# Optimization experiments

Measured on AMD Instinct MI355X. Metric: run time of the kernel, lower is better.

The kernel has to match this reference:

```python
import jax, jax.numpy as jnp
import numpy as np


def setup_inputs() -> dict:
    key = jax.random.key(0)
    k1, k2 = jax.random.split(key)
    N, DIM = 32768, 1024
    M, K, D = 8, 1024, 128  # n_quantizer, n_codeword, sub_dim
    x = jax.random.normal(k1, (N, DIM), dtype=jnp.float32)
    CodeBooks = jax.random.uniform(k2, (M, K, D), dtype=jnp.float32)  # torch.rand init
    return {"x": x, "CodeBooks": CodeBooks, "soft_rate": -1}


def reference(x, CodeBooks, soft_rate):
    # x: [N, dim]; CodeBooks: [M, K, D] with dim = M*D
    N = x.shape[0]
    M, K, D = CodeBooks.shape
    # forward detaches x before quantizing
    sx = jax.lax.stop_gradient(x).reshape(-1, M, D)  # [N, M, D]
    # squared euclidean distances for all sub-quantizers at once:
    # d2[n,m,k] = ||sx[n,m] - CB[m,k]||^2
    dots = jnp.einsum("nmd,mkd->nmk", sx, CodeBooks)          # [N, M, K]
    x2 = jnp.sum(sx * sx, axis=-1)                             # [N, M]
    c2 = jnp.sum(CodeBooks * CodeBooks, axis=-1)               # [M, K]
    d2 = x2[:, :, None] + c2[None, :, :] - 2.0 * dots          # [N, M, K]
    if soft_rate == -1:
        # argmax of -dist == argmin of squared dist (sqrt is monotone)
        idx = jnp.argmin(d2, axis=-1)                          # [N, M]
        Q = CodeBooks[jnp.arange(M)[None, :], idx]             # [N, M, D]
    else:
        dist = -jnp.sqrt(jnp.maximum(d2, 0.0))                 # -cdist, p=2
        w = jax.nn.softmax(dist * soft_rate, axis=-1)          # [N, M, K]
        Q = jnp.einsum("nmk,mkd->nmd", w, CodeBooks)           # [N, M, D]
    return Q.reshape(N, M * D)
```

## Files before the change

kernel.cpp:

```cpp
#include <hip/hip_runtime.h>
#include <stdint.h>

#define NROWS   32768
#define XDIM    1024
#define NCB     8
#define NCODE   1024
#define CDIM    128

#define CHUNK   32
#define NCHUNK  (NCODE / CHUNK)

#define NTH     256
#define ROWS_PB 128
#define RPW     32

typedef _Float16 h8 __attribute__((ext_vector_type(8)));
typedef float    f4 __attribute__((ext_vector_type(4)));

#define LO_SCALE 2048.0f
#define LO_INV   4.8828125e-4f

#define WS_HI   ((size_t)0)
#define WS_LO   ((size_t)NCB * NCODE * CDIM * 2)
#define WS_C2   ((size_t)2 * NCB * NCODE * CDIM * 2)
#define WS_NEED (WS_C2 + (size_t)NCB * NCODE * 4)

__device__ __forceinline__ void gload_lds16(const void* g, void* l) {
    __builtin_amdgcn_global_load_lds(
        (const __attribute__((address_space(1))) void*)g,
        (__attribute__((address_space(3))) void*)l, 16, 0, 0);
}

__global__ __launch_bounds__(256)
void precompute_kernel(const float* __restrict__ cb, uint8_t* __restrict__ ws)
{
    _Float16* hi = (_Float16*)(ws + WS_HI);
    _Float16* lo = (_Float16*)(ws + WS_LO);
    float*    c2 = (float*)(ws + WS_C2);

    const int idx  = blockIdx.x * 256 + threadIdx.x;
    const int g    = idx & 15;
    const int code = idx >> 4;
    const int kr   = code & 31;
    const int gs   = g ^ (kr & 7);

    const float* src = cb + (size_t)code * CDIM + gs * 8;
    float v[8];
    *(f4*)&v[0] = *(const f4*)src;
    *(f4*)&v[4] = *(const f4*)(src + 4);

    _Float16 hh[8], ll[8];
    double s = 0.0;
    #pragma unroll
    for (int i = 0; i < 8; ++i) {
        _Float16 h = (_Float16)v[i];
        float    r = v[i] - (float)h;
        hh[i] = h; ll[i] = (_Float16)(r * LO_SCALE);
        s = fma((double)v[i], (double)v[i], s);
    }
    const size_t off = (size_t)code * CDIM + g * 8;
    *(h8*)(hi + off) = *(h8*)hh;
    *(h8*)(lo + off) = *(h8*)ll;

    #pragma unroll
    for (int mask = 1; mask <= 8; mask <<= 1)
        s += __shfl_xor(s, mask, 16);
    if (g == 0) c2[code] = (float)s;
}

__global__ __launch_bounds__(NTH, 4)
void quant_fast(const float* __restrict__ x, const float* __restrict__ cb,
                const uint8_t* __restrict__ ws, float* __restrict__ out)
{
    __shared__ __align__(16) _Float16 chS[2][CHUNK][CDIM];
    __shared__ __align__(16) _Float16 clS[2][CHUNK][CDIM];
    __shared__ float  c2s[NCODE];
    __shared__ double x2p[2][ROWS_PB];
    __shared__ float  x2s[ROWS_PB];
    __shared__ int    idxs[ROWS_PB];

    const _Float16* pre_hi = (const _Float16*)(ws + WS_HI);
    const _Float16* pre_lo = (const _Float16*)(ws + WS_LO);
    const float*    c2w    = (const float*)(ws + WS_C2);

    const int t    = threadIdx.x;
    const int bid  = blockIdx.x;
    const int m    = bid >> 8;
    const int rb   = bid & 255;
    const int row0 = rb * ROWS_PB;

    const int l    = t & 63;
    const int w    = t >> 6;
    const int l15  = l & 15;
    const int lh   = l >> 4;
    const int mskr = (l & 7) * 8;

    *(f4*)&c2s[t * 4] = *(const f4*)&c2w[m * NCODE + t * 4];

    {
        const int row = t >> 1, q = t & 1;
        const float* p = x + (size_t)(row0 + row) * XDIM + m * CDIM + q * 64;
        double s0 = 0, s1 = 0;
        for (int i = 0; i < 64; i += 2) {
            double v0 = p[i], v1 = p[i + 1];
            s0 = fma(v0, v0, s0); s1 = fma(v1, v1, s1);
        }
        x2p[q][row] = s0 + s1;
    }

    h8 xh[2][4], xl[2][4];
    #pragma unroll
    for (int rs = 0; rs < 2; ++rs) {
        const float* xp = x + (size_t)(row0 + w * RPW + rs * 16 + l15) * XDIM + m * CDIM + lh * 8;
        #pragma unroll
        for (int ks = 0; ks < 4; ++ks) {
            float v[8];
            *(f4*)&v[0] = *(const f4*)(xp + ks * 32);
            *(f4*)&v[4] = *(const f4*)(xp + ks * 32 + 4);
            #pragma unroll
            for (int i = 0; i < 8; ++i) {
                _Float16 h = (_Float16)v[i];
                float    r = v[i] - (float)h;
                xh[rs][ks][i] = h;
                xl[rs][ks][i] = (_Float16)(r * LO_SCALE);
            }
        }
    }

    const size_t cbase = (size_t)m * NCODE * CDIM;
    auto stage = [&](int c, int buf) {
        const _Float16* gh = pre_hi + cbase + (size_t)(c * CHUNK + w * 8) * CDIM + l * 8;
        const _Float16* gl = pre_lo + cbase + (size_t)(c * CHUNK + w * 8) * CDIM + l * 8;
        gload_lds16(gh,            &chS[buf][w * 8][0]);
        gload_lds16(gh + 4 * CDIM, &chS[buf][w * 8 + 4][0]);
        gload_lds16(gl,            &clS[buf][w * 8][0]);
        gload_lds16(gl + 4 * CDIM, &clS[buf][w * 8 + 4][0]);
    };

    stage(0, 0);
    __syncthreads();
    if (t < ROWS_PB) x2s[t] = (float)(x2p[0][t] + x2p[1][t]);
    __syncthreads();

    float x2r[2][4];
    #pragma unroll
    for (int rs = 0; rs < 2; ++rs)
        #pragma unroll
        for (int j = 0; j < 4; ++j)
            x2r[rs][j] = x2s[w * RPW + rs * 16 + lh * 4 + j];

    float mval[2][4];
    int   midx[2][4];
    #pragma unroll
    for (int rs = 0; rs < 2; ++rs)
        #pragma unroll
        for (int j = 0; j < 4; ++j) { mval[rs][j] = 3.0e38f; midx[rs][j] = 0; }

    for (int c = 0; c < NCHUNK; ++c) {
        const int cur = c & 1;
        if (c + 1 < NCHUNK) stage(c + 1, cur ^ 1);

        #pragma unroll
        for (int cf = 0; cf < 2; ++cf) {
            const int kloc = cf * 16 + l15;
            f4 accH[2] = {{0,0,0,0},{0,0,0,0}};
            f4 accS[2] = {{0,0,0,0},{0,0,0,0}};
            #pragma unroll
            for (int ks = 0; ks < 4; ++ks) {
                const int e = (ks * 32 + lh * 8) ^ mskr;
                h8 bh = *(const h8*)&chS[cur][kloc][e];
                h8 bl = *(const h8*)&clS[cur][kloc][e];
                accH[0] = __builtin_amdgcn_mfma_f32_16x16x32_f16(xh[0][ks], bh, accH[0], 0, 0, 0);
                accH[1] = __builtin_amdgcn_mfma_f32_16x16x32_f16(xh[1][ks], bh, accH[1], 0, 0, 0);
                accS[0] = __builtin_amdgcn_mfma_f32_16x16x32_f16(xh[0][ks], bl, accS[0], 0, 0, 0);
                accS[0] = __builtin_amdgcn_mfma_f32_16x16x32_f16(xl[0][ks], bh, accS[0], 0, 0, 0);
                accS[1] = __builtin_amdgcn_mfma_f32_16x16x32_f16(xh[1][ks], bl, accS[1], 0, 0, 0);
                accS[1] = __builtin_amdgcn_mfma_f32_16x16x32_f16(xl[1][ks], bh, accS[1], 0, 0, 0);
            }
            const int   code = c * CHUNK + kloc;
            const float c2v  = c2s[code];
            #pragma unroll
            for (int rs = 0; rs < 2; ++rs)
                #pragma unroll
                for (int j = 0; j < 4; ++j) {
                    float dot = fmaf(accS[rs][j], LO_INV, accH[rs][j]);
                    float d2  = (x2r[rs][j] + c2v) - 2.0f * dot;
                    if (d2 < mval[rs][j]) { mval[rs][j] = d2; midx[rs][j] = code; }
                }
        }
        __syncthreads();
    }

    #pragma unroll
    for (int mask = 1; mask <= 8; mask <<= 1)
        #pragma unroll
        for (int rs = 0; rs < 2; ++rs)
            #pragma unroll
            for (int j = 0; j < 4; ++j) {
                float ov = __shfl_xor(mval[rs][j], mask, 64);
                int   oi = __shfl_xor(midx[rs][j], mask, 64);
                if (ov < mval[rs][j] || (ov == mval[rs][j] && oi < midx[rs][j])) {
                    mval[rs][j] = ov; midx[rs][j] = oi;
                }
            }
    if (l15 == 0)
        #pragma unroll
        for (int rs = 0; rs < 2; ++rs)
            #pragma unroll
            for (int j = 0; j < 4; ++j)
                idxs[w * RPW + rs * 16 + lh * 4 + j] = midx[rs][j];
    __syncthreads();

    {
        const int row = t >> 1, half = (t & 1) * 64;
        const float* src = cb + ((size_t)m * NCODE + idxs[row]) * CDIM + half;
        float*       dst = out + (size_t)(row0 + row) * XDIM + m * CDIM + half;
        #pragma unroll
        for (int i = 0; i < 16; ++i)
            *(f4*)(dst + i * 4) = *(const f4*)(src + i * 4);
    }
}

__global__ __launch_bounds__(512, 4)
void quant_fallback(const float* __restrict__ x, const float* __restrict__ cb,
                    float* __restrict__ out)
{
    __shared__ __align__(16) _Float16 chS[2][CHUNK][CDIM];
    __shared__ __align__(16) _Float16 clS[2][CHUNK][CDIM];
    __shared__ float  c2s[NCODE];
    __shared__ double x2p[4][ROWS_PB];
    __shared__ float  x2s[ROWS_PB];
    __shared__ int    idxs[ROWS_PB];

    const int t = threadIdx.x, bid = blockIdx.x;
    const int m = bid >> 8, rb = bid & 255, row0 = rb * ROWS_PB;
    const int l = t & 63, w = t >> 6, l15 = l & 15, lh = l >> 4;
    const int mskr = (l & 7) * 8;

    for (int rep = 0; rep < 2; ++rep) {
        int k = t + rep * 512;
        const float* p = cb + ((size_t)m * NCODE + k) * CDIM;
        double s0 = 0, s1 = 0, s2 = 0, s3 = 0;
        for (int d = 0; d < CDIM; d += 4) {
            double v0 = p[d], v1 = p[d+1], v2 = p[d+2], v3 = p[d+3];
            s0 = fma(v0,v0,s0); s1 = fma(v1,v1,s1); s2 = fma(v2,v2,s2); s3 = fma(v3,v3,s3);
        }
        c2s[k] = (float)((s0+s1)+(s2+s3));
    }
    {
        int row = t >> 2, q = t & 3;
        const float* p = x + (size_t)(row0+row)*XDIM + m*CDIM + q*32;
        double s0 = 0, s1 = 0;
        for (int i = 0; i < 32; i += 2) { double v0=p[i], v1=p[i+1]; s0=fma(v0,v0,s0); s1=fma(v1,v1,s1); }
        x2p[q][row] = s0 + s1;
    }
    h8 xh[4], xl[4];
    {
        const float* xp = x + (size_t)(row0 + w*16 + l15)*XDIM + m*CDIM + lh*8;
        #pragma unroll
        for (int ks = 0; ks < 4; ++ks) {
            float v[8];
            *(f4*)&v[0] = *(const f4*)(xp + ks*32);
            *(f4*)&v[4] = *(const f4*)(xp + ks*32 + 4);
            #pragma unroll
            for (int i = 0; i < 8; ++i) {
                _Float16 h = (_Float16)v[i]; float r = v[i] - (float)h;
                xh[ks][i] = h; xl[ks][i] = (_Float16)(r * LO_SCALE);
            }
        }
    }
    __syncthreads();
    if (t < ROWS_PB) x2s[t] = (float)((x2p[0][t]+x2p[1][t])+(x2p[2][t]+x2p[3][t]));

    const int kr = t >> 4, db = (t & 15) * 8, ew = db ^ ((kr & 7) * 8);
    auto stage_load = [&](int c, f4& a, f4& b) {
        const float* p = cb + ((size_t)m*NCODE + c*CHUNK + kr)*CDIM + db;
        a = *(const f4*)p; b = *(const f4*)(p + 4);
    };
    auto stage_write = [&](int buf, f4 a, f4 b) {
        float v[8]; *(f4*)&v[0] = a; *(f4*)&v[4] = b;
        _Float16 hh[8], ll[8];
        #pragma unroll
        for (int i = 0; i < 8; ++i) {
            _Float16 h = (_Float16)v[i]; float r = v[i] - (float)h;
            hh[i] = h; ll[i] = (_Float16)(r * LO_SCALE);
        }
        *(h8*)&chS[buf][kr][ew] = *(h8*)hh;
        *(h8*)&clS[buf][kr][ew] = *(h8*)ll;
    };

    f4 pa, pb;
    stage_load(0, pa, pb);
    stage_write(0, pa, pb);
    __syncthreads();

    float x2r[4];
    #pragma unroll
    for (int j = 0; j < 4; ++j) x2r[j] = x2s[w*16 + lh*4 + j];
    float mval[4]; int midx[4];
    #pragma unroll
    for (int j = 0; j < 4; ++j) { mval[j] = 3.0e38f; midx[j] = 0; }

    for (int c = 0; c < NCHUNK; ++c) {
        const int cur = c & 1;
        f4 na, nb;
        if (c + 1 < NCHUNK) stage_load(c + 1, na, nb);
        #pragma unroll
        for (int cf = 0; cf < 2; ++cf) {
            const int kloc = cf*16 + l15;
            f4 accH = {0,0,0,0}, accS = {0,0,0,0};
            #pragma unroll
            for (int ks = 0; ks < 4; ++ks) {
                const int e = (ks*32 + lh*8) ^ mskr;
                h8 bh = *(const h8*)&chS[cur][kloc][e];
                h8 bl = *(const h8*)&clS[cur][kloc][e];
                accH = __builtin_amdgcn_mfma_f32_16x16x32_f16(xh[ks], bh, accH, 0, 0, 0);
                accS = __builtin_amdgcn_mfma_f32_16x16x32_f16(xh[ks], bl, accS, 0, 0, 0);
                accS = __builtin_amdgcn_mfma_f32_16x16x32_f16(xl[ks], bh, accS, 0, 0, 0);
            }
            const int code = c*CHUNK + kloc;
            const float c2v = c2s[code];
            #pragma unroll
            for (int j = 0; j < 4; ++j) {
                float dot = fmaf(accS[j], LO_INV, accH[j]);
                float d2 = (x2r[j] + c2v) - 2.0f*dot;
                if (d2 < mval[j]) { mval[j] = d2; midx[j] = code; }
            }
        }
        if (c + 1 < NCHUNK) stage_write((c + 1) & 1, na, nb);
        __syncthreads();
    }
    #pragma unroll
    for (int mask = 1; mask <= 8; mask <<= 1)
        #pragma unroll
        for (int j = 0; j < 4; ++j) {
            float ov = __shfl_xor(mval[j], mask, 64);
            int   oi = __shfl_xor(midx[j], mask, 64);
            if (ov < mval[j] || (ov == mval[j] && oi < midx[j])) { mval[j] = ov; midx[j] = oi; }
        }
    if (l15 == 0)
        #pragma unroll
        for (int j = 0; j < 4; ++j) idxs[w*16 + lh*4 + j] = midx[j];
    __syncthreads();
    {
        const int row = t >> 2, qd = (t & 3) * 32;
        const float* src = cb + ((size_t)m*NCODE + idxs[row])*CDIM + qd;
        float* dst = out + (size_t)(row0+row)*XDIM + m*CDIM + qd;
        #pragma unroll
        for (int i = 0; i < 8; ++i) *(f4*)(dst + i*4) = *(const f4*)(src + i*4);
    }
}

extern "C" void kernel_launch(void* const* d_in, const int* in_sizes, int n_in,
                              void* d_out, int out_size, void* d_ws, size_t ws_size,
                              hipStream_t stream) {
    const float* x   = (const float*)d_in[0];
    const float* cb  = (const float*)d_in[1];
    float*       out = (float*)d_out;
    if (ws_size >= WS_NEED && d_ws != nullptr) {
        precompute_kernel<<<dim3(512), dim3(256), 0, stream>>>(cb, (uint8_t*)d_ws);
        quant_fast<<<dim3(2048), dim3(NTH), 0, stream>>>(x, cb, (const uint8_t*)d_ws, out);
    } else {
        quant_fallback<<<dim3(2048), dim3(512), 0, stream>>>(x, cb, out);
    }
}
```

Baseline: 330.6 us.

## Double rows per block, triple-buffer codebook staging, and remap block order

Result: faster. 300.1 us (-9.2%).

```diff
diff --git a/kernel.cpp b/kernel.cpp
--- a/kernel.cpp
+++ b/kernel.cpp
@@ -9,10 +9,11 @@
 
 #define CHUNK   32
 #define NCHUNK  (NCODE / CHUNK)
+#define NBUF    3
 
 #define NTH     256
-#define ROWS_PB 128
-#define RPW     32
+#define ROWS_PB 256
+#define RPW     64
 
 typedef _Float16 h8 __attribute__((ext_vector_type(8)));
 typedef float    f4 __attribute__((ext_vector_type(4)));
@@ -68,14 +69,13 @@
     if (g == 0) c2[code] = (float)s;
 }
 
-__global__ __launch_bounds__(NTH, 4)
+__global__ __launch_bounds__(NTH, 2)
 void quant_fast(const float* __restrict__ x, const float* __restrict__ cb,
                 const uint8_t* __restrict__ ws, float* __restrict__ out)
 {
-    __shared__ __align__(16) _Float16 chS[2][CHUNK][CDIM];
-    __shared__ __align__(16) _Float16 clS[2][CHUNK][CDIM];
+    __shared__ __align__(16) _Float16 chS[NBUF][CHUNK][CDIM];
+    __shared__ __align__(16) _Float16 clS[NBUF][CHUNK][CDIM];
     __shared__ float  c2s[NCODE];
-    __shared__ double x2p[2][ROWS_PB];
     __shared__ float  x2s[ROWS_PB];
     __shared__ int    idxs[ROWS_PB];
 
@@ -84,9 +84,9 @@
     const float*    c2w    = (const float*)(ws + WS_C2);
 
     const int t    = threadIdx.x;
-    const int bid  = blockIdx.x;
-    const int m    = bid >> 8;
-    const int rb   = bid & 255;
+    const int wgid = (blockIdx.x & 7) * 128 + (blockIdx.x >> 3);
+    const int m    = wgid >> 7;
+    const int rb   = wgid & 127;
     const int row0 = rb * ROWS_PB;
 
     const int l    = t & 63;
@@ -95,39 +95,8 @@
     const int lh   = l >> 4;
     const int mskr = (l & 7) * 8;
 
-    *(f4*)&c2s[t * 4] = *(const f4*)&c2w[m * NCODE + t * 4];
-
-    {
-        const int row = t >> 1, q = t & 1;
-        const float* p = x + (size_t)(row0 + row) * XDIM + m * CDIM + q * 64;
-        double s0 = 0, s1 = 0;
-        for (int i = 0; i < 64; i += 2) {
-            double v0 = p[i], v1 = p[i + 1];
-            s0 = fma(v0, v0, s0); s1 = fma(v1, v1, s1);
-        }
-        x2p[q][row] = s0 + s1;
-    }
-
-    h8 xh[2][4], xl[2][4];
-    #pragma unroll
-    for (int rs = 0; rs < 2; ++rs) {
-        const float* xp = x + (size_t)(row0 + w * RPW + rs * 16 + l15) * XDIM + m * CDIM + lh * 8;
-        #pragma unroll
-        for (int ks = 0; ks < 4; ++ks) {
-            float v[8];
-            *(f4*)&v[0] = *(const f4*)(xp + ks * 32);
-            *(f4*)&v[4] = *(const f4*)(xp + ks * 32 + 4);
-            #pragma unroll
-            for (int i = 0; i < 8; ++i) {
-                _Float16 h = (_Float16)v[i];
-                float    r = v[i] - (float)h;
-                xh[rs][ks][i] = h;
-                xl[rs][ks][i] = (_Float16)(r * LO_SCALE);
-            }
-        }
-    }
-
     const size_t cbase = (size_t)m * NCODE * CDIM;
+
     auto stage = [&](int c, int buf) {
         const _Float16* gh = pre_hi + cbase + (size_t)(c * CHUNK + w * 8) * CDIM + l * 8;
         const _Float16* gl = pre_lo + cbase + (size_t)(c * CHUNK + w * 8) * CDIM + l * 8;
@@ -136,51 +105,77 @@
         gload_lds16(gl,            &clS[buf][w * 8][0]);
         gload_lds16(gl + 4 * CDIM, &clS[buf][w * 8 + 4][0]);
     };
-
     stage(0, 0);
-    __syncthreads();
-    if (t < ROWS_PB) x2s[t] = (float)(x2p[0][t] + x2p[1][t]);
-    __syncthreads();
-
-    float x2r[2][4];
-    #pragma unroll
-    for (int rs = 0; rs < 2; ++rs)
+    stage(1, 1);
+
+    *(f4*)&c2s[t * 4] = *(const f4*)&c2w[m * NCODE + t * 4];
+
+    h8 xh[4][4], xl[4][4];
+    #pragma unroll
+    for (int rs = 0; rs < 4; ++rs) {
+        const float* xp = x + (size_t)(row0 + w * RPW + rs * 16 + l15) * XDIM + m * CDIM + lh * 8;
+        double s = 0.0;
+        #pragma unroll
+        for (int ks = 0; ks < 4; ++ks) {
+            float v[8];
+            *(f4*)&v[0] = *(const f4*)(xp + ks * 32);
+            *(f4*)&v[4] = *(const f4*)(xp + ks * 32 + 4);
+            #pragma unroll
+            for (int i = 0; i < 8; ++i) {
+                _Float16 h = (_Float16)v[i];
+                float    r = v[i] - (float)h;
+                xh[rs][ks][i] = h;
+                xl[rs][ks][i] = (_Float16)(r * LO_SCALE);
+                s = fma((double)v[i], (double)v[i], s);
+            }
+        }
+        s += __shfl_xor(s, 16, 64);
+        s += __shfl_xor(s, 32, 64);
+        if (lh == 0) x2s[w * RPW + rs * 16 + l15] = (float)s;
+    }
+
+    asm volatile("s_waitcnt vmcnt(4) lgkmcnt(0)" ::: "memory");
+    asm volatile("s_barrier" ::: "memory");
+
+    float x2r[4][4];
+    #pragma unroll
+    for (int rs = 0; rs < 4; ++rs)
         #pragma unroll
         for (int j = 0; j < 4; ++j)
             x2r[rs][j] = x2s[w * RPW + rs * 16 + lh * 4 + j];
 
-    float mval[2][4];
-    int   midx[2][4];
-    #pragma unroll
-    for (int rs = 0; rs < 2; ++rs)
+    float mval[4][4];
+    int   midx[4][4];
+    #pragma unroll
+    for (int rs = 0; rs < 4; ++rs)
         #pragma unroll
         for (int j = 0; j < 4; ++j) { mval[rs][j] = 3.0e38f; midx[rs][j] = 0; }
 
+    int cur = 0, nxt = 2;
     for (int c = 0; c < NCHUNK; ++c) {
-        const int cur = c & 1;
-        if (c + 1 < NCHUNK) stage(c + 1, cur ^ 1);
+        if (c + 2 < NCHUNK) stage(c + 2, nxt);
 
         #pragma unroll
         for (int cf = 0; cf < 2; ++cf) {
             const int kloc = cf * 16 + l15;
-            f4 accH[2] = {{0,0,0,0},{0,0,0,0}};
-            f4 accS[2] = {{0,0,0,0},{0,0,0,0}};
+            f4 accH[4] = {{0,0,0,0},{0,0,0,0},{0,0,0,0},{0,0,0,0}};
+            f4 accS[4] = {{0,0,0,0},{0,0,0,0},{0,0,0,0},{0,0,0,0}};
             #pragma unroll
             for (int ks = 0; ks < 4; ++ks) {
                 const int e = (ks * 32 + lh * 8) ^ mskr;
                 h8 bh = *(const h8*)&chS[cur][kloc][e];
                 h8 bl = *(const h8*)&clS[cur][kloc][e];
-                accH[0] = __builtin_amdgcn_mfma_f32_16x16x32_f16(xh[0][ks], bh, accH[0], 0, 0, 0);
-                accH[1] = __builtin_amdgcn_mfma_f32_16x16x32_f16(xh[1][ks], bh, accH[1], 0, 0, 0);
-                accS[0] = __builtin_amdgcn_mfma_f32_16x16x32_f16(xh[0][ks], bl, accS[0], 0, 0, 0);
-                accS[0] = __builtin_amdgcn_mfma_f32_16x16x32_f16(xl[0][ks], bh, accS[0], 0, 0, 0);
-                accS[1] = __builtin_amdgcn_mfma_f32_16x16x32_f16(xh[1][ks], bl, accS[1], 0, 0, 0);
-                accS[1] = __builtin_amdgcn_mfma_f32_16x16x32_f16(xl[1][ks], bh, accS[1], 0, 0, 0);
+                #pragma unroll
+                for (int rs = 0; rs < 4; ++rs) {
+                    accH[rs] = __builtin_amdgcn_mfma_f32_16x16x32_f16(xh[rs][ks], bh, accH[rs], 0, 0, 0);
+                    accS[rs] = __builtin_amdgcn_mfma_f32_16x16x32_f16(xh[rs][ks], bl, accS[rs], 0, 0, 0);
+                    accS[rs] = __builtin_amdgcn_mfma_f32_16x16x32_f16(xl[rs][ks], bh, accS[rs], 0, 0, 0);
+                }
             }
             const int   code = c * CHUNK + kloc;
             const float c2v  = c2s[code];
             #pragma unroll
-            for (int rs = 0; rs < 2; ++rs)
+            for (int rs = 0; rs < 4; ++rs)
                 #pragma unroll
                 for (int j = 0; j < 4; ++j) {
                     float dot = fmaf(accS[rs][j], LO_INV, accH[rs][j]);
@@ -188,13 +183,22 @@
                     if (d2 < mval[rs][j]) { mval[rs][j] = d2; midx[rs][j] = code; }
                 }
         }
-        __syncthreads();
+
+        if (c < NCHUNK - 2) {
+            asm volatile("s_waitcnt vmcnt(4)" ::: "memory");
+        } else {
+            asm volatile("s_waitcnt vmcnt(0)" ::: "memory");
+        }
+        asm volatile("s_barrier" ::: "memory");
+
+        cur = (cur == NBUF - 1) ? 0 : cur + 1;
+        nxt = (nxt == NBUF - 1) ? 0 : nxt + 1;
     }
 
     #pragma unroll
     for (int mask = 1; mask <= 8; mask <<= 1)
         #pragma unroll
-        for (int rs = 0; rs < 2; ++rs)
+        for (int rs = 0; rs < 4; ++rs)
             #pragma unroll
             for (int j = 0; j < 4; ++j) {
                 float ov = __shfl_xor(mval[rs][j], mask, 64);
@@ -205,14 +209,16 @@
             }
     if (l15 == 0)
         #pragma unroll
-        for (int rs = 0; rs < 2; ++rs)
+        for (int rs = 0; rs < 4; ++rs)
             #pragma unroll
             for (int j = 0; j < 4; ++j)
                 idxs[w * RPW + rs * 16 + lh * 4 + j] = midx[rs][j];
     __syncthreads();
 
-    {
-        const int row = t >> 1, half = (t & 1) * 64;
+    #pragma unroll
+    for (int pass = 0; pass < 2; ++pass) {
+        const int row  = pass * 128 + (t >> 1);
+        const int half = (t & 1) * 64;
         const float* src = cb + ((size_t)m * NCODE + idxs[row]) * CDIM + half;
         float*       dst = out + (size_t)(row0 + row) * XDIM + m * CDIM + half;
         #pragma unroll
@@ -228,12 +234,12 @@
     __shared__ __align__(16) _Float16 chS[2][CHUNK][CDIM];
     __shared__ __align__(16) _Float16 clS[2][CHUNK][CDIM];
     __shared__ float  c2s[NCODE];
-    __shared__ double x2p[4][ROWS_PB];
-    __shared__ float  x2s[ROWS_PB];
-    __shared__ int    idxs[ROWS_PB];
+    __shared__ double x2p[4][128];
+    __shared__ float  x2s[128];
+    __shared__ int    idxs[128];
 
     const int t = threadIdx.x, bid = blockIdx.x;
-    const int m = bid >> 8, rb = bid & 255, row0 = rb * ROWS_PB;
+    const int m = bid >> 8, rb = bid & 255, row0 = rb * 128;
     const int l = t & 63, w = t >> 6, l15 = l & 15, lh = l >> 4;
     const int mskr = (l & 7) * 8;
 
@@ -270,7 +276,7 @@
         }
     }
     __syncthreads();
-    if (t < ROWS_PB) x2s[t] = (float)((x2p[0][t]+x2p[1][t])+(x2p[2][t]+x2p[3][t]));
+    if (t < 128) x2s[t] = (float)((x2p[0][t]+x2p[1][t])+(x2p[2][t]+x2p[3][t]));
 
     const int kr = t >> 4, db = (t & 15) * 8, ew = db ^ ((kr & 7) * 8);
     auto stage_load = [&](int c, f4& a, f4& b) {
@@ -359,7 +365,7 @@
     float*       out = (float*)d_out;
     if (ws_size >= WS_NEED && d_ws != nullptr) {
         precompute_kernel<<<dim3(512), dim3(256), 0, stream>>>(cb, (uint8_t*)d_ws);
-        quant_fast<<<dim3(2048), dim3(NTH), 0, stream>>>(x, cb, (const uint8_t*)d_ws, out);
+        quant_fast<<<dim3(NCB * (NROWS / ROWS_PB)), dim3(NTH), 0, stream>>>(x, cb, (const uint8_t*)d_ws, out);
     } else {
         quant_fallback<<<dim3(2048), dim3(512), 0, stream>>>(x, cb, out);
     }
```

## Double rows per block, fuse x-norm into fp16 split, interleave codebook block order

Applied to the files above, without the earlier changes.

Result: faster. 300.6 us (median of 2 runs) (-9.1%).

```diff
diff --git a/kernel.cpp b/kernel.cpp
--- a/kernel.cpp
+++ b/kernel.cpp
@@ -10,8 +10,8 @@
 #define CHUNK   32
 #define NCHUNK  (NCODE / CHUNK)
 
-#define NTH     256
-#define ROWS_PB 128
+#define NTH     512
+#define ROWS_PB 256
 #define RPW     32
 
 typedef _Float16 h8 __attribute__((ext_vector_type(8)));
@@ -75,7 +75,6 @@
     __shared__ __align__(16) _Float16 chS[2][CHUNK][CDIM];
     __shared__ __align__(16) _Float16 clS[2][CHUNK][CDIM];
     __shared__ float  c2s[NCODE];
-    __shared__ double x2p[2][ROWS_PB];
     __shared__ float  x2s[ROWS_PB];
     __shared__ int    idxs[ROWS_PB];
 
@@ -84,9 +83,8 @@
     const float*    c2w    = (const float*)(ws + WS_C2);
 
     const int t    = threadIdx.x;
-    const int bid  = blockIdx.x;
-    const int m    = bid >> 8;
-    const int rb   = bid & 255;
+    const int m    = blockIdx.x & 7;
+    const int rb   = blockIdx.x >> 3;
     const int row0 = rb * ROWS_PB;
 
     const int l    = t & 63;
@@ -95,23 +93,24 @@
     const int lh   = l >> 4;
     const int mskr = (l & 7) * 8;
 
-    *(f4*)&c2s[t * 4] = *(const f4*)&c2w[m * NCODE + t * 4];
-
-    {
-        const int row = t >> 1, q = t & 1;
-        const float* p = x + (size_t)(row0 + row) * XDIM + m * CDIM + q * 64;
-        double s0 = 0, s1 = 0;
-        for (int i = 0; i < 64; i += 2) {
-            double v0 = p[i], v1 = p[i + 1];
-            s0 = fma(v0, v0, s0); s1 = fma(v1, v1, s1);
-        }
-        x2p[q][row] = s0 + s1;
-    }
+    const size_t cbase = (size_t)m * NCODE * CDIM;
+
+    auto stage = [&](int c, int buf) {
+        const _Float16* gh = pre_hi + cbase + (size_t)(c * CHUNK + w * 4) * CDIM + l * 8;
+        const _Float16* gl = pre_lo + cbase + (size_t)(c * CHUNK + w * 4) * CDIM + l * 8;
+        gload_lds16(gh, &chS[buf][w * 4][0]);
+        gload_lds16(gl, &clS[buf][w * 4][0]);
+    };
+
+    stage(0, 0);
+
+    if (t < 256) *(f4*)&c2s[t * 4] = *(const f4*)&c2w[m * NCODE + t * 4];
 
     h8 xh[2][4], xl[2][4];
     #pragma unroll
     for (int rs = 0; rs < 2; ++rs) {
         const float* xp = x + (size_t)(row0 + w * RPW + rs * 16 + l15) * XDIM + m * CDIM + lh * 8;
+        double s = 0.0;
         #pragma unroll
         for (int ks = 0; ks < 4; ++ks) {
             float v[8];
@@ -123,23 +122,14 @@
                 float    r = v[i] - (float)h;
                 xh[rs][ks][i] = h;
                 xl[rs][ks][i] = (_Float16)(r * LO_SCALE);
-            }
-        }
-    }
-
-    const size_t cbase = (size_t)m * NCODE * CDIM;
-    auto stage = [&](int c, int buf) {
-        const _Float16* gh = pre_hi + cbase + (size_t)(c * CHUNK + w * 8) * CDIM + l * 8;
-        const _Float16* gl = pre_lo + cbase + (size_t)(c * CHUNK + w * 8) * CDIM + l * 8;
-        gload_lds16(gh,            &chS[buf][w * 8][0]);
-        gload_lds16(gh + 4 * CDIM, &chS[buf][w * 8 + 4][0]);
-        gload_lds16(gl,            &clS[buf][w * 8][0]);
-        gload_lds16(gl + 4 * CDIM, &clS[buf][w * 8 + 4][0]);
-    };
-
-    stage(0, 0);
-    __syncthreads();
-    if (t < ROWS_PB) x2s[t] = (float)(x2p[0][t] + x2p[1][t]);
+                s = fma((double)v[i], (double)v[i], s);
+            }
+        }
+        s += __shfl_xor(s, 16, 64);
+        s += __shfl_xor(s, 32, 64);
+        if (lh == 0) x2s[w * RPW + rs * 16 + l15] = (float)s;
+    }
+
     __syncthreads();
 
     float x2r[2][4];
@@ -212,7 +202,8 @@
     __syncthreads();
 
     {
-        const int row = t >> 1, half = (t & 1) * 64;
+        const int row  = t >> 1;
+        const int half = (t & 1) * 64;
         const float* src = cb + ((size_t)m * NCODE + idxs[row]) * CDIM + half;
         float*       dst = out + (size_t)(row0 + row) * XDIM + m * CDIM + half;
         #pragma unroll
@@ -228,12 +219,12 @@
     __shared__ __align__(16) _Float16 chS[2][CHUNK][CDIM];
     __shared__ __align__(16) _Float16 clS[2][CHUNK][CDIM];
     __shared__ float  c2s[NCODE];
-    __shared__ double x2p[4][ROWS_PB];
-    __shared__ float  x2s[ROWS_PB];
-    __shared__ int    idxs[ROWS_PB];
+    __shared__ double x2p[4][128];
+    __shared__ float  x2s[128];
+    __shared__ int    idxs[128];
 
     const int t = threadIdx.x, bid = blockIdx.x;
-    const int m = bid >> 8, rb = bid & 255, row0 = rb * ROWS_PB;
+    const int m = bid >> 8, rb = bid & 255, row0 = rb * 128;
     const int l = t & 63, w = t >> 6, l15 = l & 15, lh = l >> 4;
     const int mskr = (l & 7) * 8;
 
@@ -270,7 +261,7 @@
         }
     }
     __syncthreads();
-    if (t < ROWS_PB) x2s[t] = (float)((x2p[0][t]+x2p[1][t])+(x2p[2][t]+x2p[3][t]));
+    if (t < 128) x2s[t] = (float)((x2p[0][t]+x2p[1][t])+(x2p[2][t]+x2p[3][t]));
 
     const int kr = t >> 4, db = (t & 15) * 8, ew = db ^ ((kr & 7) * 8);
     auto stage_load = [&](int c, f4& a, f4& b) {
@@ -359,7 +350,8 @@
     float*       out = (float*)d_out;
     if (ws_size >= WS_NEED && d_ws != nullptr) {
         precompute_kernel<<<dim3(512), dim3(256), 0, stream>>>(cb, (uint8_t*)d_ws);
-        quant_fast<<<dim3(2048), dim3(NTH), 0, stream>>>(x, cb, (const uint8_t*)d_ws, out);
+        quant_fast<<<dim3(NCB * (NROWS / ROWS_PB)), dim3(NTH), 0, stream>>>(
+            x, cb, (const uint8_t*)d_ws, out);
     } else {
         quant_fallback<<<dim3(2048), dim3(512), 0, stream>>>(x, cb, out);
     }
```
